# Optimization experiments

Hardware: AMD Instinct MI355X
Metric: run time of the kernel (lower is better)

Reference implementation:

```python
import jax, jax.numpy as jnp
import numpy as np

NUM_HEADS = 16
HEAD_DIM = 64
WINDOW_SIZE = 512
D_MODEL = NUM_HEADS * HEAD_DIM
B, S = 2, 2048


def setup_inputs() -> dict:
    key = jax.random.key(0)
    ks = jax.random.split(key, 5)
    w_scale = 1.0 / np.sqrt(D_MODEL)
    return {
        "x": jax.random.normal(ks[0], (B, S, D_MODEL), dtype=jnp.float32),
        "Wq": jax.random.normal(ks[1], (D_MODEL, D_MODEL), dtype=jnp.float32) * w_scale,
        "bq": jnp.zeros((D_MODEL,), dtype=jnp.float32),
        "Wk": jax.random.normal(ks[2], (D_MODEL, D_MODEL), dtype=jnp.float32) * w_scale,
        "bk": jnp.zeros((D_MODEL,), dtype=jnp.float32),
        "Wv": jax.random.normal(ks[3], (D_MODEL, D_MODEL), dtype=jnp.float32) * w_scale,
        "bv": jnp.zeros((D_MODEL,), dtype=jnp.float32),
        "Wo": jax.random.normal(ks[4], (D_MODEL, D_MODEL), dtype=jnp.float32) * w_scale,
        "bo": jnp.zeros((D_MODEL,), dtype=jnp.float32),
    }


def reference(x, Wq, bq, Wk, bk, Wv, bv, Wo, bo):
    batch, seq_len, _ = x.shape

    def split_heads(t):  # [B,S,D] -> [B,H,S,hd]
        return t.reshape(batch, seq_len, NUM_HEADS, HEAD_DIM).transpose(0, 2, 1, 3)

    q = split_heads(x @ Wq + bq)
    k = split_heads(x @ Wk + bk)
    v = split_heads(x @ Wv + bv)

    # sliding-window band mask combined with causal mask: keep j in (i - window, i]
    pos = jnp.arange(seq_len)
    diff = pos[:, None] - pos[None, :]  # [S,S]
    keep = (diff >= 0) & (diff < WINDOW_SIZE)  # band & causal
    keep = keep[None, None, :, :]  # [1,1,S,S]

    scale = 1.0 / jnp.sqrt(jnp.asarray(HEAD_DIM, dtype=q.dtype))
    scores = jnp.einsum('bhid,bhjd->bhij', q, k) * scale
    scores = jnp.where(keep, scores, jnp.asarray(-1e9, dtype=scores.dtype))
    attention_weights = jax.nn.softmax(scores, axis=-1)  # [B,H,S,S]

    attended = jnp.einsum('bhij,bhjd->bhid', attention_weights, v)
    attended = attended.transpose(0, 2, 1, 3).reshape(batch, seq_len, D_MODEL)
    output = attended @ Wo + bo
    return (output, attention_weights)
```

## Files before the change

kernel.cpp:

```cpp
#include <hip/hip_runtime.h>
#include <cstdint>
#include <cstddef>

#define NH  16
#define HD  64
#define DM  1024
#define SB  2048
#define WIN 512

typedef _Float16 half8  __attribute__((ext_vector_type(8)));
typedef _Float16 half4  __attribute__((ext_vector_type(4)));
typedef float    f32x4  __attribute__((ext_vector_type(4)));

#define GLL16(gp, lp) __builtin_amdgcn_global_load_lds( \
    (const __attribute__((address_space(1))) void*)(gp), \
    (__attribute__((address_space(3))) void*)(lp), 16, 0, 0)

__device__ __forceinline__ void zero_fill_role(float* zbase, int plane0, int nplanes,
                                               int fb, int nfb) {
  const int nrows = nplanes << 11;
  const f32x4 z4 = {0.f, 0.f, 0.f, 0.f};
  const int tid = threadIdx.x;
  const int step = blockDim.x * 4;
  for (int rr = fb; rr < nrows; rr += nfb) {
    const int bh = plane0 + (rr >> 11), i = rr & 2047;
    float* rowp = zbase + ((size_t)bh << 22) + ((size_t)i << 11);
    const int t0i = i & ~15;
    const int par = (t0i >> 4) & 1;
    int lo = t0i - 512 - 16 * par; if (lo < 0) lo = 0;
    int hi = t0i + 32 + 16 * par;  if (hi > SB) hi = SB;
    for (int c = tid * 4; c < lo; c += step)
      __builtin_nontemporal_store(z4, (f32x4*)(rowp + c));
    for (int c = hi + tid * 4; c < SB; c += step)
      __builtin_nontemporal_store(z4, (f32x4*)(rowp + c));
  }
}

__global__ void k_pre(const float* __restrict__ x,
                      const float* __restrict__ Wq, const float* __restrict__ Wk,
                      const float* __restrict__ Wv, const float* __restrict__ Wo,
                      _Float16* __restrict__ xh, _Float16* __restrict__ Wt) {
  __shared__ float t[64][68];
  const int bid = blockIdx.x, tid = threadIdx.x;
  if (bid < 2048) {
    const int i = (bid * 256 + tid) * 8;
    const float4 a = *(const float4*)(x + i);
    const float4 b = *(const float4*)(x + i + 4);
    half8 o = { (_Float16)a.x, (_Float16)a.y, (_Float16)a.z, (_Float16)a.w,
                (_Float16)b.x, (_Float16)b.y, (_Float16)b.z, (_Float16)b.w };
    *(half8*)(xh + i) = o;
    return;
  }
  const int tt = bid - 2048;
  const int z = tt >> 8, r2 = tt & 255;
  const int k0 = (r2 >> 4) * 64, n0 = (r2 & 15) * 64;
  const float* src = (z == 0) ? Wq : (z == 1) ? Wk : (z == 2) ? Wv : Wo;
  _Float16* dst = Wt + (size_t)z * DM * DM;
  #pragma unroll
  for (int i = 0; i < 4; ++i) {
    const int idx = i * 1024 + tid * 4;
    const int r = idx >> 6, c = idx & 63;
    const float4 v = *(const float4*)(src + (size_t)(k0 + r) * DM + n0 + c);
    *(float4*)(&t[r][c]) = v;
  }
  __syncthreads();
  #pragma unroll
  for (int i = 0; i < 4; ++i) {
    const int idx = i * 1024 + tid * 4;
    const int nr = idx >> 6, kc = idx & 63;
    half4 o = { (_Float16)t[kc + 0][nr], (_Float16)t[kc + 1][nr],
                (_Float16)t[kc + 2][nr], (_Float16)t[kc + 3][nr] };
    *(half4*)(dst + (size_t)(n0 + nr) * DM + k0 + kc) = o;
  }
}

template<bool F32OUT>
__global__ __launch_bounds__(256, 4) void k_gemm(
    const _Float16* __restrict__ A, const _Float16* __restrict__ Wt,
    const float* __restrict__ b0, const float* __restrict__ b1, const float* __restrict__ b2,
    void* __restrict__ outv, _Float16* __restrict__ Vt, float scale0,
    float* __restrict__ zbase, int plane0, int nplanes)
{
  __shared__ _Float16 As[128 * 64];
  __shared__ _Float16 Bs[128 * 64];
  if (blockIdx.x >= 32) {
    const int FBn = gridDim.x - 32;
    const int fb  = (blockIdx.x - 32) + FBn * (blockIdx.y + gridDim.y * blockIdx.z);
    zero_fill_role(zbase, plane0, nplanes, fb, FBn * gridDim.y * gridDim.z);
    return;
  }

  const int z = blockIdx.z;
  const _Float16* Wz = Wt + (size_t)z * DM * DM;
  const float* bias = (z == 0) ? b0 : (z == 1) ? b1 : b2;
  const float scale = (z == 0) ? scale0 : 1.0f;
  const int m0 = blockIdx.x * 128, n0 = blockIdx.y * 128;
  const int tid = threadIdx.x, lane = tid & 63, wid = tid >> 6;
  const int g = lane >> 4, li = lane & 15;
  const int wr = (wid & 1) * 64, wc = (wid >> 1) * 64;

  f32x4 acc[4][4] = {};

  for (int kt = 0; kt < 16; ++kt) {
    const int kb = kt * 64;
    #pragma unroll
    for (int i = 0; i < 4; ++i) {
      const int c = wid + 4 * i;
      const int off = c * 1024 + lane * 16;
      const int r = off >> 7;
      const int cb = off & 127;
      const int sc_ = cb ^ ((r & 7) << 4);
      GLL16(A  + (size_t)(m0 + r) * DM + kb + (sc_ >> 1), (char*)As + c * 1024);
      GLL16(Wz + (size_t)(n0 + r) * DM + kb + (sc_ >> 1), (char*)Bs + c * 1024);
    }
    __syncthreads();
    #pragma unroll
    for (int kk = 0; kk < 2; ++kk) {
      half8 bf[4];
      #pragma unroll
      for (int ni = 0; ni < 4; ++ni) {
        const int r = wc + ni * 16 + li;
        const int cbyte = (kk * 64 + g * 16) ^ ((r & 7) << 4);
        bf[ni] = *(const half8*)((const char*)Bs + r * 128 + cbyte);
      }
      #pragma unroll
      for (int mi = 0; mi < 4; ++mi) {
        const int r = wr + mi * 16 + li;
        const int cbyte = (kk * 64 + g * 16) ^ ((r & 7) << 4);
        const half8 af = *(const half8*)((const char*)As + r * 128 + cbyte);
        #pragma unroll
        for (int ni = 0; ni < 4; ++ni)
          acc[mi][ni] = __builtin_amdgcn_mfma_f32_16x16x32_f16(af, bf[ni], acc[mi][ni], 0, 0, 0);
      }
    }
    __syncthreads();
  }

  float bv[4];
  #pragma unroll
  for (int ni = 0; ni < 4; ++ni) bv[ni] = bias[n0 + wc + ni * 16 + li];

  if (!F32OUT && z == 2) {
    #pragma unroll
    for (int mi = 0; mi < 4; ++mi)
      #pragma unroll
      for (int ni = 0; ni < 4; ++ni) {
        const int col = n0 + wc + ni * 16 + li;
        const int h2 = col >> 6, d = col & 63;
        const int row0 = m0 + wr + mi * 16 + g * 4;
        const int bb = row0 >> 11, s0 = row0 & 2047;
        half4 o = { (_Float16)(acc[mi][ni][0] + bv[ni]), (_Float16)(acc[mi][ni][1] + bv[ni]),
                    (_Float16)(acc[mi][ni][2] + bv[ni]), (_Float16)(acc[mi][ni][3] + bv[ni]) };
        *(half4*)(Vt + (size_t)((bb * NH + h2) * HD + d) * SB + s0) = o;
      }
    return;
  }

  #pragma unroll
  for (int mi = 0; mi < 4; ++mi)
    #pragma unroll
    for (int ni = 0; ni < 4; ++ni)
      #pragma unroll
      for (int reg = 0; reg < 4; ++reg) {
        const int row = m0 + wr + mi * 16 + g * 4 + reg;
        const int col = n0 + wc + ni * 16 + li;
        const float v = (acc[mi][ni][reg] + bv[ni]) * scale;
        if (F32OUT) ((float*)outv)[(size_t)row * DM + col] = v;
        else ((_Float16*)outv + (size_t)z * 4096 * 1024)[(size_t)row * DM + col] = (_Float16)v;
      }
}

__global__ __launch_bounds__(256, 8) void k_attn(
    const _Float16* __restrict__ Q, const _Float16* __restrict__ K,
    const _Float16* __restrict__ Vt, float* __restrict__ Wout,
    _Float16* __restrict__ attb, int plane0, int nplanes)
{
  __shared__ float sred[4][16];
  __shared__ f32x4 ored[3][64][4];
  if (blockIdx.x >= 128) {
    const int FBn = gridDim.x - 128;
    const int fb  = (blockIdx.x - 128) + FBn * (blockIdx.y + gridDim.y * blockIdx.z);
    zero_fill_role(Wout, plane0, nplanes, fb, FBn * gridDim.y * gridDim.z);
    return;
  }

  const int b = blockIdx.z, h = blockIdx.y;
  const int tid = threadIdx.x, lane = tid & 63, wid = tid >> 6;
  const int g = lane >> 4, li = lane & 15;
  const int t0 = blockIdx.x * 16;

  half8 qf[2];
  #pragma unroll
  for (int kk = 0; kk < 2; ++kk)
    qf[kk] = *(const half8*)(Q + (size_t)(b * SB + t0 + li) * DM + h * HD + kk * 32 + g * 8);

  const int ktq = t0 >> 4;
  const int kt_lo = ktq - 32;
  const int d1 = kt_lo & 1;
  const int ktA0 = kt_lo - d1;
  const _Float16* kb_ = K + (size_t)b * SB * DM + (size_t)h * HD;
  const int i = t0 + li;

  const int c_base = (wid == 0) ? 0 : (wid == 1) ? 5 : (wid == 2) ? (9 + d1) : (13 + d1);
  const int c_cnt  = (wid == 0) ? 5 : (wid == 1) ? (4 + d1) : 4;
  const int it_lo  = 2 * c_base - d1;
  const int it_n   = 2 * c_cnt;

  half4 pp[10] = {};
  float s = 0.f;
  #pragma unroll
  for (int itl = 0; itl < 10; ++itl) {
    const int it = it_lo + itl;
    if (itl >= it_n || it < 0 || it > 32) continue;
    const int kt = kt_lo + it;
    if (kt < 0) continue;
    f32x4 a = {0.f, 0.f, 0.f, 0.f};
    #pragma unroll
    for (int kk = 0; kk < 2; ++kk) {
      half8 kf = *(const half8*)(kb_ + (size_t)(kt * 16 + li) * DM + kk * 32 + g * 8);
      a = __builtin_amdgcn_mfma_f32_16x16x32_f16(kf, qf[kk], a, 0, 0, 0);
    }
    float p0 = exp2f(a[0]), p1 = exp2f(a[1]), p2 = exp2f(a[2]), p3 = exp2f(a[3]);
    if (it == 0) {
      p0 = (g * 4 + 0 > li) ? p0 : 0.f;
      p1 = (g * 4 + 1 > li) ? p1 : 0.f;
      p2 = (g * 4 + 2 > li) ? p2 : 0.f;
      p3 = (g * 4 + 3 > li) ? p3 : 0.f;
    }
    if (it == 32) {
      p0 = (g * 4 + 0 <= li) ? p0 : 0.f;
      p1 = (g * 4 + 1 <= li) ? p1 : 0.f;
      p2 = (g * 4 + 2 <= li) ? p2 : 0.f;
      p3 = (g * 4 + 3 <= li) ? p3 : 0.f;
    }
    s += (p0 + p1) + (p2 + p3);
    pp[itl] = (half4){(_Float16)p0, (_Float16)p1, (_Float16)p2, (_Float16)p3};
  }

  s += __shfl_xor(s, 16);
  s += __shfl_xor(s, 32);
  if (lane < 16) sred[wid][lane] = s;
  __syncthreads();
  const float rinv = 1.0f / (sred[0][li] + sred[1][li] + sred[2][li] + sred[3][li]);

  const _Float16* vb = Vt + (size_t)(b * NH + h) * HD * SB;
  float* wb = Wout + (size_t)(b * NH + h) * SB * SB;
  f32x4 oacc[4] = {};
  #pragma unroll
  for (int cl = 0; cl < 5; ++cl) {
    if (cl >= c_cnt) continue;
    const int ktA = ktA0 + 2 * (c_base + cl);
    if (ktA + 1 < 0) continue;
    float pAf[4], pBf[4];
    #pragma unroll
    for (int r = 0; r < 4; ++r) { pAf[r] = (float)pp[2 * cl][r]; pBf[r] = (float)pp[2 * cl + 1][r]; }
    const int jA0 = ktA * 16 + g * 4;
    if (jA0 >= 0 && jA0 < SB) {
      f32x4 w = {pAf[0] * rinv, pAf[1] * rinv, pAf[2] * rinv, pAf[3] * rinv};
      __builtin_nontemporal_store(w, (f32x4*)(wb + (size_t)i * SB + jA0));
    }
    const int jB0 = jA0 + 16;
    if (jB0 >= 0 && jB0 < SB) {
      f32x4 w = {pBf[0] * rinv, pBf[1] * rinv, pBf[2] * rinv, pBf[3] * rinv};
      __builtin_nontemporal_store(w, (f32x4*)(wb + (size_t)i * SB + jB0));
    }
    half8 pa;
    #pragma unroll
    for (int c8 = 0; c8 < 8; ++c8) {
      const int srcl = ((2 * (g & 1) + (c8 >> 2)) << 4) + li;
      const float va  = __shfl(pAf[c8 & 3], srcl);
      const float vb2 = __shfl(pBf[c8 & 3], srcl);
      pa[c8] = (_Float16)(g < 2 ? va : vb2);
    }
    int jb = ktA * 16 + g * 8;
    jb = jb < 0 ? 0 : (jb > SB - 8 ? SB - 8 : jb);
    #pragma unroll
    for (int dt = 0; dt < 4; ++dt) {
      half8 vf = *(const half8*)(vb + (size_t)(dt * 16 + li) * SB + jb);
      oacc[dt] = __builtin_amdgcn_mfma_f32_16x16x32_f16(pa, vf, oacc[dt], 0, 0, 0);
    }
  }

  if (wid > 0) {
    #pragma unroll
    for (int dt = 0; dt < 4; ++dt) ored[wid - 1][lane][dt] = oacc[dt];
  }
  __syncthreads();
  if (wid == 0) {
    #pragma unroll
    for (int dt = 0; dt < 4; ++dt)
      oacc[dt] += ored[0][lane][dt] + ored[1][lane][dt] + ored[2][lane][dt];
    #pragma unroll
    for (int dt = 0; dt < 4; ++dt)
      #pragma unroll
      for (int r = 0; r < 4; ++r) {
        const float rr = __shfl(rinv, g * 4 + r);
        attb[(size_t)(b * SB + t0 + g * 4 + r) * DM + h * HD + dt * 16 + li] =
            (_Float16)(oacc[dt][r] * rr);
      }
  }
}

extern "C" void kernel_launch(void* const* d_in, const int* in_sizes, int n_in,
                              void* d_out, int out_size, void* d_ws, size_t ws_size,
                              hipStream_t stream) {
  (void)in_sizes; (void)n_in; (void)out_size; (void)ws_size;
  const float* x  = (const float*)d_in[0];
  const float* Wq = (const float*)d_in[1];
  const float* bq = (const float*)d_in[2];
  const float* Wk = (const float*)d_in[3];
  const float* bk = (const float*)d_in[4];
  const float* Wv = (const float*)d_in[5];
  const float* bv = (const float*)d_in[6];
  const float* Wo = (const float*)d_in[7];
  const float* bo = (const float*)d_in[8];

  char* ws = (char*)d_ws;
  _Float16* xh   = (_Float16*)(ws);
  _Float16* Wt   = (_Float16*)(ws + (size_t)8  * 1048576);
  _Float16* QKV  = (_Float16*)(ws + (size_t)16 * 1048576);
  _Float16* Vt   = (_Float16*)(ws + (size_t)32 * 1048576);
  _Float16* attb = (_Float16*)(ws + (size_t)40 * 1048576);

  float* out   = (float*)d_out;
  float* Wattn = out + (size_t)2 * SB * DM;

  const float qscale = 0.125f * 1.4426950408889634f;
  const _Float16* Kp = QKV + (size_t)4096 * 1024;

  k_pre<<<dim3(3072), dim3(256), 0, stream>>>(x, Wq, Wk, Wv, Wo, xh, Wt);
  k_gemm<false><<<dim3(40, 8, 3), dim3(256), 0, stream>>>(xh, Wt, bq, bk, bv, (void*)QKV, Vt, qscale, Wattn, 0, 12);
  k_attn<<<dim3(144, 16, 2), dim3(256), 0, stream>>>(QKV, Kp, Vt, Wattn, attb, 12, 12);
  k_gemm<true><<<dim3(64, 8, 1), dim3(256), 0, stream>>>(attb, Wt + (size_t)3 * DM * DM, bo, bo, bo, (void*)out, nullptr, 1.0f, Wattn, 24, 8);
}
```

Measured before the change: 169.1 us.

## Stage attention weights in LDS for row-contiguous stores and swizzle query tiles

Unnormalized probabilities are written to a shared-memory tile, then each wave writes whole rows of the attention-weight matrix with contiguous 16-byte nontemporal stores, replacing the scattered per-lane stores. This targets poor write coalescing on the large fp32 weight output. The query tile index is also permuted across blocks to spread concurrently running blocks along the sequence, and launch bounds drop from 8 to 4 blocks per CU to make room for the extra ~18KB of LDS, which may lower occupancy.

Result: no change. 166.2 us (-1.7%).

```diff
diff --git a/kernel.cpp b/kernel.cpp
--- a/kernel.cpp
+++ b/kernel.cpp
@@ -170,13 +170,14 @@
       }
 }
 
-__global__ __launch_bounds__(256, 8) void k_attn(
+__global__ __launch_bounds__(256, 4) void k_attn(
     const _Float16* __restrict__ Q, const _Float16* __restrict__ K,
     const _Float16* __restrict__ Vt, float* __restrict__ Wout,
     _Float16* __restrict__ attb, int plane0, int nplanes)
 {
   __shared__ float sred[4][16];
   __shared__ f32x4 ored[3][64][4];
+  __shared__ _Float16 pw[16][584];
   if (blockIdx.x >= 128) {
     const int FBn = gridDim.x - 128;
     const int fb  = (blockIdx.x - 128) + FBn * (blockIdx.y + gridDim.y * blockIdx.z);
@@ -187,19 +188,18 @@
   const int b = blockIdx.z, h = blockIdx.y;
   const int tid = threadIdx.x, lane = tid & 63, wid = tid >> 6;
   const int g = lane >> 4, li = lane & 15;
-  const int t0 = blockIdx.x * 16;
+  const int qt = ((blockIdx.x & 7) << 4) | (blockIdx.x >> 3);
+  const int t0 = qt * 16;
 
   half8 qf[2];
   #pragma unroll
   for (int kk = 0; kk < 2; ++kk)
     qf[kk] = *(const half8*)(Q + (size_t)(b * SB + t0 + li) * DM + h * HD + kk * 32 + g * 8);
 
-  const int ktq = t0 >> 4;
-  const int kt_lo = ktq - 32;
+  const int kt_lo = qt - 32;
   const int d1 = kt_lo & 1;
   const int ktA0 = kt_lo - d1;
   const _Float16* kb_ = K + (size_t)b * SB * DM + (size_t)h * HD;
-  const int i = t0 + li;
 
   const int c_base = (wid == 0) ? 0 : (wid == 1) ? 5 : (wid == 2) ? (9 + d1) : (13 + d1);
   const int c_cnt  = (wid == 0) ? 5 : (wid == 1) ? (4 + d1) : 4;
@@ -210,10 +210,14 @@
   float s = 0.f;
   #pragma unroll
   for (int itl = 0; itl < 10; ++itl) {
+    if (itl >= it_n) continue;
     const int it = it_lo + itl;
-    if (itl >= it_n || it < 0 || it > 32) continue;
     const int kt = kt_lo + it;
-    if (kt < 0) continue;
+    const int scol = (it + d1) * 16 + g * 4;
+    if (it < 0 || it > 32 || kt < 0) {
+      *(half4*)(&pw[li][scol]) = (half4){(_Float16)0.f, (_Float16)0.f, (_Float16)0.f, (_Float16)0.f};
+      continue;
+    }
     f32x4 a = {0.f, 0.f, 0.f, 0.f};
     #pragma unroll
     for (int kk = 0; kk < 2; ++kk) {
@@ -234,7 +238,9 @@
       p3 = (g * 4 + 3 <= li) ? p3 : 0.f;
     }
     s += (p0 + p1) + (p2 + p3);
-    pp[itl] = (half4){(_Float16)p0, (_Float16)p1, (_Float16)p2, (_Float16)p3};
+    half4 ph = {(_Float16)p0, (_Float16)p1, (_Float16)p2, (_Float16)p3};
+    pp[itl] = ph;
+    *(half4*)(&pw[li][scol]) = ph;
   }
 
   s += __shfl_xor(s, 16);
@@ -243,8 +249,31 @@
   __syncthreads();
   const float rinv = 1.0f / (sred[0][li] + sred[1][li] + sred[2][li] + sred[3][li]);
 
+  {
+    float* wb = Wout + (size_t)(b * NH + h) * SB * SB;
+    const int W4 = 136 + 8 * d1;
+    const int cs = ktA0 * 16;
+    #pragma unroll
+    for (int rr = 0; rr < 4; ++rr) {
+      const int r_ = wid * 4 + rr;
+      const float rv = 1.0f / (sred[0][r_] + sred[1][r_] + sred[2][r_] + sred[3][r_]);
+      float* dst = wb + (size_t)(t0 + r_) * SB;
+      #pragma unroll
+      for (int p = 0; p < 3; ++p) {
+        const int idx = p * 64 + lane;
+        if (idx < W4) {
+          const int gc = cs + 4 * idx;
+          if (gc >= 0 && gc < SB) {
+            const half4 hv = *(const half4*)(&pw[r_][4 * idx]);
+            f32x4 w = {(float)hv[0] * rv, (float)hv[1] * rv, (float)hv[2] * rv, (float)hv[3] * rv};
+            __builtin_nontemporal_store(w, (f32x4*)(dst + gc));
+          }
+        }
+      }
+    }
+  }
+
   const _Float16* vb = Vt + (size_t)(b * NH + h) * HD * SB;
-  float* wb = Wout + (size_t)(b * NH + h) * SB * SB;
   f32x4 oacc[4] = {};
   #pragma unroll
   for (int cl = 0; cl < 5; ++cl) {
@@ -254,16 +283,6 @@
     float pAf[4], pBf[4];
     #pragma unroll
     for (int r = 0; r < 4; ++r) { pAf[r] = (float)pp[2 * cl][r]; pBf[r] = (float)pp[2 * cl + 1][r]; }
-    const int jA0 = ktA * 16 + g * 4;
-    if (jA0 >= 0 && jA0 < SB) {
-      f32x4 w = {pAf[0] * rinv, pAf[1] * rinv, pAf[2] * rinv, pAf[3] * rinv};
-      __builtin_nontemporal_store(w, (f32x4*)(wb + (size_t)i * SB + jA0));
-    }
-    const int jB0 = jA0 + 16;
-    if (jB0 >= 0 && jB0 < SB) {
-      f32x4 w = {pBf[0] * rinv, pBf[1] * rinv, pBf[2] * rinv, pBf[3] * rinv};
-      __builtin_nontemporal_store(w, (f32x4*)(wb + (size_t)i * SB + jB0));
-    }
     half8 pa;
     #pragma unroll
     for (int c8 = 0; c8 < 8; ++c8) {
```
